# Optimization experiments

Measured on AMD Instinct MI355X. Metric: run time of the kernel, lower is better.

The kernel has to match this reference:

```python
import jax, jax.numpy as jnp
import numpy as np

SEQ_LEN = 2048; WIN = 32; NW = SEQ_LEN // WIN; FEAT = 16
H = 64; E = 128; NH = 4; OUT = 5; B = 256; MAXN = 2


def setup_inputs() -> dict:
    key = jax.random.key(0)
    ks = jax.random.split(key, 20)
    n = lambda k, shape, s=0.05: jax.random.normal(k, shape, dtype=jnp.float32) * s
    return {
        'x': n(ks[0], (B, SEQ_LEN, FEAT), 1.0),
        # bidirectional LSTM (torch gate order i,f,g,o)
        'w_ih_f': n(ks[1], (4 * H, FEAT)), 'w_hh_f': n(ks[2], (4 * H, H)),
        'b_ih_f': jnp.zeros((4 * H,)), 'b_hh_f': jnp.zeros((4 * H,)),
        'w_ih_b': n(ks[3], (4 * H, FEAT)), 'w_hh_b': n(ks[4], (4 * H, H)),
        'b_ih_b': jnp.zeros((4 * H,)), 'b_hh_b': jnp.zeros((4 * H,)),
        # self-attention on bi-LSTM output (embed_dim = 2H = E)
        'sa_in_w': n(ks[5], (3 * E, E)), 'sa_in_b': jnp.zeros((3 * E,)),
        'sa_out_w': n(ks[6], (E, E)), 'sa_out_b': jnp.zeros((E,)),
        # projection 2H -> embed_dim
        'proj_w': n(ks[7], (E, 2 * H)), 'proj_b': jnp.zeros((E,)),
        # per-window cross-attention blocks (stacked along NW)
        'ca_in_w': n(ks[8], (NW, 3 * E, E)), 'ca_in_b': jnp.zeros((NW, 3 * E)),
        'ca_out_w': n(ks[9], (NW, E, E)), 'ca_out_b': jnp.zeros((NW, E)),
        'ln_g': jnp.ones((NW, E)), 'ln_b': jnp.zeros((NW, E)),
        # final dense heads
        'fd1_w': n(ks[10], (64, E * NW)), 'fd1_b': jnp.zeros((64,)),
        'fd2_w': n(ks[11], (OUT, 64)), 'fd2_b': jnp.zeros((OUT,)),
    }


def _lstm_dir(x, w_ih, w_hh, b_ih, b_hh):
    # x: [N, T, F] -> hidden states [N, T, H]
    N = x.shape[0]
    Hh = w_hh.shape[1]
    xp = jnp.einsum('ntf,gf->ntg', x, w_ih) + b_ih + b_hh  # [N,T,4H]

    def step(carry, xt):
        h, c = carry
        g = xt + h @ w_hh.T
        i, f, gg, o = jnp.split(g, 4, axis=-1)
        i = jax.nn.sigmoid(i); f = jax.nn.sigmoid(f)
        gg = jnp.tanh(gg); o = jax.nn.sigmoid(o)
        c = f * c + i * gg
        h = o * jnp.tanh(c)
        return (h, c), h

    init = (jnp.zeros((N, Hh), x.dtype), jnp.zeros((N, Hh), x.dtype))
    _, hs = jax.lax.scan(step, init, jnp.swapaxes(xp, 0, 1))
    return jnp.swapaxes(hs, 0, 1)


def _bilstm(x, wif, whf, bif, bhf, wib, whb, bib, bhb):
    fwd = _lstm_dir(x, wif, whf, bif, bhf)
    bwd = _lstm_dir(x[:, ::-1], wib, whb, bib, bhb)[:, ::-1]
    return jnp.concatenate([fwd, bwd], axis=-1)  # [N, T, 2H]


def _mha(q_x, kv_x, in_w, in_b, out_w, out_b, nh):
    # torch nn.MultiheadAttention (batch_first, eval mode)
    Ed = q_x.shape[-1]; d = Ed // nh
    q = q_x @ in_w[:Ed].T + in_b[:Ed]
    k = kv_x @ in_w[Ed:2 * Ed].T + in_b[Ed:2 * Ed]
    v = kv_x @ in_w[2 * Ed:].T + in_b[2 * Ed:]
    sh = lambda t: t.reshape(t.shape[0], t.shape[1], nh, d)
    q, k, v = sh(q), sh(k), sh(v)
    s = jnp.einsum('nqhd,nkhd->nhqk', q, k) / jnp.asarray(np.sqrt(d), q.dtype)
    a = jax.nn.softmax(s, axis=-1)
    o = jnp.einsum('nhqk,nkhd->nqhd', a, v).reshape(q_x.shape[0], q_x.shape[1], Ed)
    return o @ out_w.T + out_b


def _layernorm(x, g, b, eps=1e-5):
    m = x.mean(-1, keepdims=True)
    v = ((x - m) ** 2).mean(-1, keepdims=True)
    return (x - m) / jnp.sqrt(v + eps) * g + b


def reference(x, w_ih_f, w_hh_f, b_ih_f, b_hh_f, w_ih_b, w_hh_b, b_ih_b, b_hh_b,
              sa_in_w, sa_in_b, sa_out_w, sa_out_b, proj_w, proj_b,
              ca_in_w, ca_in_b, ca_out_w, ca_out_b, ln_g, ln_b,
              fd1_w, fd1_b, fd2_w, fd2_b):
    Bsz = x.shape[0]
    xw = x[:, :NW * WIN].reshape(Bsz * NW, WIN, FEAT)
    # bi-LSTM + self-attention (dropout = identity in eval)
    lo = _bilstm(xw, w_ih_f, w_hh_f, b_ih_f, b_hh_f, w_ih_b, w_hh_b, b_ih_b, b_hh_b)
    sa = _mha(lo, lo, sa_in_w, sa_in_b, sa_out_w, sa_out_b, NH)
    p = sa @ proj_w.T + proj_b
    pooled = p.mean(axis=1).reshape(Bsz, NW, E)
    # per-window local cross-attention with distinct weights per window
    outs = []
    for ci in range(NW):
        left = max(0, ci - MAXN); right = min(NW, ci + MAXN + 1)
        idx = np.array([i for i in range(left, right) if i != ci])
        ctx = pooled[:, idx, :]           # [B, <=2*MAXN, E]
        cen = pooled[:, ci:ci + 1, :]     # [B, 1, E]
        a = _mha(cen, ctx, ca_in_w[ci], ca_in_b[ci], ca_out_w[ci], ca_out_b[ci], NH)
        outs.append(_layernorm(a + cen, ln_g[ci], ln_b[ci]))
    seq = jnp.concatenate(outs, axis=1).reshape(Bsz, NW * E)
    h1 = jax.nn.relu(seq @ fd1_w.T + fd1_b)
    out = h1 @ fd2_w.T + fd2_b            # [B, OUT]
    return out
```

## Files before the change

### kernel.cpp

```cpp
#include <hip/hip_runtime.h>


typedef __attribute__((ext_vector_type(8))) short bf16x8;
typedef __attribute__((ext_vector_type(4))) float f32x4;

__device__ __forceinline__ unsigned short f2bf(float f) {
    union { float f; unsigned int u; } v; v.f = f;
    unsigned int u = v.u;
    return (unsigned short)((u + 0x7FFFu + ((u >> 16) & 1u)) >> 16);
}
__device__ __forceinline__ float dot4_(float4 a, float4 b) {
    return a.x*b.x + a.y*b.y + a.z*b.z + a.w*b.w;
}
__device__ __forceinline__ bf16x8 f2bf8(float4 a, float4 b) {
    bf16x8 o;
    o[0] = (short)f2bf(a.x); o[1] = (short)f2bf(a.y);
    o[2] = (short)f2bf(a.z); o[3] = (short)f2bf(a.w);
    o[4] = (short)f2bf(b.x); o[5] = (short)f2bf(b.y);
    o[6] = (short)f2bf(b.z); o[7] = (short)f2bf(b.w);
    return o;
}
__device__ __forceinline__ float bflo(unsigned u){ union{unsigned u;float f;}v; v.u=u<<16; return v.f; }
__device__ __forceinline__ float bfhi(unsigned u){ union{unsigned u;float f;}v; v.u=u&0xffff0000u; return v.f; }
#define KEEP(f) { uint4* _p = (uint4*)&(f); \
    asm volatile("" : "+v"(_p->x), "+v"(_p->y), "+v"(_p->z), "+v"(_p->w)); }

#define W_SA_IN   0
#define W_SA_OUT  49152
#define W_PROJ    65536
#define W_IH_F    81920
#define W_IH_B    86016
#define W_HH_F    90112
#define W_HH_B    106496
#define W_CA_IN   122880
#define W_CA_OUT  3268608
#define NBF_SMALL 122880
#define NBF_FULL  4317184

__global__ __launch_bounds__(256)
void prep_weights(const float* __restrict__ sa_in_w, const float* __restrict__ sa_out_w,
                  const float* __restrict__ proj_w,
                  const float* __restrict__ w_ih_f, const float* __restrict__ w_ih_b,
                  const float* __restrict__ w_hh_f, const float* __restrict__ w_hh_b,
                  const float* __restrict__ ca_in_w, const float* __restrict__ ca_out_w,
                  unsigned short* __restrict__ wbf, int n)
{
    for (int i = blockIdx.x * 256 + threadIdx.x; i < n; i += gridDim.x * 256) {
        float v;
        if (i < W_SA_OUT)       v = sa_in_w[i];
        else if (i < W_PROJ)    v = sa_out_w[i - W_SA_OUT];
        else if (i < W_IH_F)    v = proj_w[i - W_PROJ];
        else if (i < W_IH_B)    v = w_ih_f[i - W_IH_F];
        else if (i < W_HH_F)    v = w_ih_b[i - W_IH_B];
        else if (i < W_HH_B)    v = w_hh_f[i - W_HH_F];
        else if (i < W_CA_IN)   v = w_hh_b[i - W_HH_B];
        else if (i < W_CA_OUT)  v = ca_in_w[i - W_CA_IN];
        else                    v = ca_out_w[i - W_CA_OUT];
        wbf[i] = f2bf(v);
    }
}

__global__ __launch_bounds__(128)
void prep_w2(const float* __restrict__ sa_out_w, const float* __restrict__ sa_out_b,
             const float* __restrict__ proj_w, const float* __restrict__ proj_b,
             unsigned short* __restrict__ w2bf, float* __restrict__ b2f)
{
    __shared__ float pw[128];
    const int e = blockIdx.x, j = threadIdx.x;
    pw[j] = proj_w[e * 128 + j];
    __syncthreads();
    float acc = 0.f;
    #pragma unroll 8
    for (int k = 0; k < 128; ++k) acc += pw[k] * sa_out_w[k * 128 + j];
    w2bf[e * 128 + j] = f2bf(acc);
    if (j == 0) {
        float b = proj_b[e];
        for (int k = 0; k < 128; ++k) b += pw[k] * sa_out_b[k];
        b2f[e] = b;
    }
}

#define HB 0
#define XS 9216
#define LSTM_SM 25856

__global__ __launch_bounds__(512)
void lstm_kernel(const float* __restrict__ x,
    const float* __restrict__ b_ih_f, const float* __restrict__ b_hh_f,
    const float* __restrict__ b_ih_b, const float* __restrict__ b_hh_b,
    const unsigned short* __restrict__ wbf,
    unsigned short* __restrict__ lo, int win0)
{
    __shared__ __align__(16) unsigned short sm[LSTM_SM];
    const int tid = threadIdx.x;
    const int gbase = win0 + blockIdx.x * 32;
    const int bb = gbase >> 6;
    const int wi0 = gbase & 63;

    for (int i = tid; i < 9216; i += 512) sm[HB + i] = 0;
    #pragma unroll
    for (int i = 0; i < 2; ++i) {
        const int p = tid + i * 512;
        const int win = p >> 5, t = p & 31;
        const float4* src = (const float4*)(x + ((size_t)bb * 2048 + (wi0 + win) * 32 + t) * 16);
        const float4 v0 = src[0], v1 = src[1], v2 = src[2], v3 = src[3];
        *(bf16x8*)&sm[XS + win * 520 + t * 16]     = f2bf8(v0, v1);
        *(bf16x8*)&sm[XS + win * 520 + t * 16 + 8] = f2bf8(v2, v3);
    }
    __syncthreads();

    const int w = tid >> 6, lane = tid & 63;
    const int dir = w >> 2, wd = w & 3;
    const int quad = lane >> 4, n16 = lane & 15;
    const bf16x8 zf = {};

    const unsigned short* whh = wbf + (dir ? W_HH_B : W_HH_F);
    const unsigned short* wih = wbf + (dir ? W_IH_B : W_IH_F);
    const float* bi = dir ? b_ih_b : b_ih_f;
    const float* bh = dir ? b_hh_b : b_hh_f;

    bf16x8 wf[4][2], xf[4];
    float bias[4];
    #pragma unroll
    for (int j = 0; j < 4; ++j) {
        const int g = 64 * j + wd * 16 + n16;
        wf[j][0] = *(const bf16x8*)(whh + g * 64 + quad * 8);
        wf[j][1] = *(const bf16x8*)(whh + g * 64 + 32 + quad * 8);
        KEEP(wf[j][0]); KEEP(wf[j][1]);
        xf[j] = (quad < 2) ? *(const bf16x8*)(wih + g * 16 + quad * 8) : zf;
        KEEP(xf[j]);
        bias[j] = bi[g] + bh[g];
    }
    float c[2][4] = {};
    const size_t loB = (size_t)blockIdx.x * 32;

    for (int s = 0; s < 32; ++s) {
        const int t = dir ? (31 - s) : s;
        const int cur = s & 1, nxt = cur ^ 1;
        #pragma unroll
        for (int mt = 0; mt < 2; ++mt) {
            const int hb = HB + ((cur * 2 + dir) * 32 + mt * 16 + n16) * 72;
            const bf16x8 ah0 = *(const bf16x8*)&sm[hb + quad * 8];
            const bf16x8 ah1 = *(const bf16x8*)&sm[hb + 32 + quad * 8];
            const bf16x8 ax = (quad < 2)
                ? *(const bf16x8*)&sm[XS + (mt * 16 + n16) * 520 + t * 16 + quad * 8] : zf;
            f32x4 ga[4];
            #pragma unroll
            for (int j = 0; j < 4; ++j) {
                f32x4 acc = {bias[j], bias[j], bias[j], bias[j]};
                acc = __builtin_amdgcn_mfma_f32_16x16x32_bf16(ah0, wf[j][0], acc, 0, 0, 0);
                acc = __builtin_amdgcn_mfma_f32_16x16x32_bf16(ah1, wf[j][1], acc, 0, 0, 0);
                acc = __builtin_amdgcn_mfma_f32_16x16x32_bf16(ax,  xf[j],   acc, 0, 0, 0);
                ga[j] = acc;
            }
            #pragma unroll
            for (int r = 0; r < 4; ++r) {
                const float iv = 1.f / (1.f + __expf(-ga[0][r]));
                const float fv = 1.f / (1.f + __expf(-ga[1][r]));
                const float gv = 2.f / (1.f + __expf(-2.f * ga[2][r])) - 1.f;
                const float ov = 1.f / (1.f + __expf(-ga[3][r]));
                c[mt][r] = fv * c[mt][r] + iv * gv;
                const float hv = ov * (2.f / (1.f + __expf(-2.f * c[mt][r])) - 1.f);
                sm[HB + ((nxt * 2 + dir) * 32 + mt * 16 + quad * 4 + r) * 72 + wd * 16 + n16]
                    = f2bf(hv);
            }
        }
        __syncthreads();
        {
            const int win = tid >> 4, part = tid & 15;
            const int d2 = part >> 3, u0 = (part & 7) * 8;
            const int t2 = d2 ? (31 - s) : s;
            const uint4 hv = *(const uint4*)&sm[HB + ((nxt * 2 + d2) * 32 + win) * 72 + u0];
            *(uint4*)(lo + ((loB + win) * 32 + t2) * 128 + d2 * 64 + u0) = hv;
        }
    }
}

#define LO16 0
#define Q16  4352
#define K16  8704
#define VT16 13056
#define SM16_TOTAL 18176

__global__ __launch_bounds__(512)
void attn_kernel(const unsigned short* __restrict__ wbf,
    const float* __restrict__ sa_in_b,
    const unsigned short* __restrict__ w2bf, const float* __restrict__ b2f,
    const unsigned short* __restrict__ lo,
    float* __restrict__ pooled, int win0)
{
    __shared__ __align__(16) unsigned short sm16[SM16_TOTAL];
    const int tid = threadIdx.x;

    {
        const uint4 v = *(const uint4*)(lo + (size_t)blockIdx.x * 4096 + tid * 8);
        const int t = tid >> 4, e0 = (tid & 15) * 8;
        *(uint4*)&sm16[LO16 + t * 136 + e0] = v;
    }
    __syncthreads();

    const int w    = tid >> 6;
    const int lane = tid & 63;
    const int quad = lane >> 4;
    const int m16  = lane & 15;
    const unsigned short* wqkv = wbf + W_SA_IN;
    const f32x4 z = {0.f, 0.f, 0.f, 0.f};

    {
        bf16x8 afr[2][4];
        #pragma unroll
        for (int mt = 0; mt < 2; ++mt)
            #pragma unroll
            for (int kk = 0; kk < 4; ++kk)
                afr[mt][kk] = *(const bf16x8*)&sm16[LO16 + (mt*16 + m16)*136 + kk*32 + quad*8];
        #pragma unroll
        for (int i = 0; i < 3; ++i) {
            const int nt = w * 3 + i;
            const int e = nt * 16 + m16;
            bf16x8 bfr[4];
            #pragma unroll
            for (int kk = 0; kk < 4; ++kk)
                bfr[kk] = *(const bf16x8*)(wqkv + (size_t)e*128 + kk*32 + quad*8);
            f32x4 acc0 = z, acc1 = z;
            #pragma unroll
            for (int kk = 0; kk < 4; ++kk) {
                acc0 = __builtin_amdgcn_mfma_f32_16x16x32_bf16(afr[0][kk], bfr[kk], acc0, 0, 0, 0);
                acc1 = __builtin_amdgcn_mfma_f32_16x16x32_bf16(afr[1][kk], bfr[kk], acc1, 0, 0, 0);
            }
            const float bias = sa_in_b[e];
            #pragma unroll
            for (int r = 0; r < 4; ++r) {
                const int r0 = quad*4 + r, r1 = 16 + r0;
                const unsigned short h0 = f2bf(acc0[r] + bias);
                const unsigned short h1 = f2bf(acc1[r] + bias);
                if (e < 128) {
                    sm16[Q16 + r0*136 + e] = h0;
                    sm16[Q16 + r1*136 + e] = h1;
                } else if (e < 256) {
                    sm16[K16 + r0*136 + (e-128)] = h0;
                    sm16[K16 + r1*136 + (e-128)] = h1;
                } else {
                    sm16[VT16 + (e-256)*40 + r0] = h0;
                    sm16[VT16 + (e-256)*40 + r1] = h1;
                }
            }
        }
    }
    __syncthreads();

    {
        const int h  = w >> 1;
        const int mt = w & 1;
        const bf16x8 aq  = *(const bf16x8*)&sm16[Q16 + (mt*16 + m16)*136 + h*32 + quad*8];
        const bf16x8 bk0 = *(const bf16x8*)&sm16[K16 + (m16)*136      + h*32 + quad*8];
        const bf16x8 bk1 = *(const bf16x8*)&sm16[K16 + (16 + m16)*136 + h*32 + quad*8];
        f32x4 s0 = __builtin_amdgcn_mfma_f32_16x16x32_bf16(aq, bk0, z, 0, 0, 0);
        f32x4 s1 = __builtin_amdgcn_mfma_f32_16x16x32_bf16(aq, bk1, z, 0, 0, 0);
        const float scale = 0.17677669529663687f;
        #pragma unroll
        for (int r = 0; r < 4; ++r) {
            const int rowt = mt*16 + quad*4 + r;
            sm16[Q16 + rowt*136 + h*32 + m16]      = f2bf(__expf(s0[r] * scale));
            sm16[Q16 + rowt*136 + h*32 + 16 + m16] = f2bf(__expf(s1[r] * scale));
        }
        const bf16x8 ap  = *(const bf16x8*)&sm16[Q16 + (mt*16 + m16)*136 + h*32 + quad*8];
        bf16x8 ones;
        #pragma unroll
        for (int j = 0; j < 8; ++j) ones[j] = (short)0x3F80;
        const f32x4 sums = __builtin_amdgcn_mfma_f32_16x16x32_bf16(ap, ones, z, 0, 0, 0);
        const bf16x8 bv0 = *(const bf16x8*)&sm16[VT16 + (h*32 + m16)*40      + quad*8];
        const bf16x8 bv1 = *(const bf16x8*)&sm16[VT16 + (h*32 + 16 + m16)*40 + quad*8];
        f32x4 o0 = __builtin_amdgcn_mfma_f32_16x16x32_bf16(ap, bv0, z, 0, 0, 0);
        f32x4 o1 = __builtin_amdgcn_mfma_f32_16x16x32_bf16(ap, bv1, z, 0, 0, 0);
        float cs0 = 0.f, cs1 = 0.f;
        #pragma unroll
        for (int r = 0; r < 4; ++r) {
            const float inv = 1.f / sums[r];
            cs0 += o0[r] * inv;
            cs1 += o1[r] * inv;
        }
        cs0 += __shfl_xor(cs0, 16, 64); cs0 += __shfl_xor(cs0, 32, 64);
        cs1 += __shfl_xor(cs1, 16, 64); cs1 += __shfl_xor(cs1, 32, 64);
        float* osum = (float*)&sm16[LO16];
        if (quad == 0) {
            osum[mt*128 + h*32 + m16]      = cs0;
            osum[mt*128 + h*32 + 16 + m16] = cs1;
        }
    }
    __syncthreads();

    if (tid < 128) {
        const float* osum = (const float*)&sm16[LO16];
        float acc = b2f[tid];
        const unsigned short* wrow = w2bf + tid * 128;
        #pragma unroll
        for (int j0 = 0; j0 < 128; j0 += 8) {
            const uint4 u = *(const uint4*)(wrow + j0);
            acc += (osum[j0+0] + osum[128+j0+0]) * 0.03125f * bflo(u.x);
            acc += (osum[j0+1] + osum[128+j0+1]) * 0.03125f * bfhi(u.x);
            acc += (osum[j0+2] + osum[128+j0+2]) * 0.03125f * bflo(u.y);
            acc += (osum[j0+3] + osum[128+j0+3]) * 0.03125f * bfhi(u.y);
            acc += (osum[j0+4] + osum[128+j0+4]) * 0.03125f * bflo(u.z);
            acc += (osum[j0+5] + osum[128+j0+5]) * 0.03125f * bfhi(u.z);
            acc += (osum[j0+6] + osum[128+j0+6]) * 0.03125f * bflo(u.w);
            acc += (osum[j0+7] + osum[128+j0+7]) * 0.03125f * bfhi(u.w);
        }
        pooled[((size_t)(win0 + blockIdx.x)) * 128 + tid] = acc;
    }
}

__global__ __launch_bounds__(256)
void cross_mfma_kernel(const float* __restrict__ pooled,
    const unsigned short* __restrict__ wbf,
    const float* __restrict__ ca_in_b, const float* __restrict__ ca_out_b,
    const float* __restrict__ ln_g, const float* __restrict__ ln_b,
    float* __restrict__ seq)
{
    __shared__ __align__(16) float cenf[16 * 128];
    __shared__ __align__(16) unsigned short cenb[16 * 136];
    __shared__ __align__(16) unsigned short ctxb[64 * 136];
    __shared__ __align__(16) unsigned short qb[16 * 136];
    __shared__ __align__(16) unsigned short kb[64 * 136];
    __shared__ __align__(16) unsigned short ob[16 * 136];
    __shared__ float attr[256];
    __shared__ float att[256];

    const int blk = blockIdx.x;
    const int ci = blk >> 4;
    const int ch = blk & 15;
    const int tid = threadIdx.x;
    const int w = tid >> 6, lane = tid & 63, quad = lane >> 4, n16 = lane & 15;

    const int left  = (ci - 2 > 0) ? ci - 2 : 0;
    const int right = (ci + 3 < 64) ? ci + 3 : 64;
    const int nc = right - left - 1;

    {
        const int b = tid >> 4, e0 = (tid & 15) * 8;
        const float4* src = (const float4*)(pooled + ((size_t)(ch*16 + b)*64 + ci)*128 + e0);
        const float4 v0 = src[0], v1 = src[1];
        *(float4*)&cenf[b*128 + e0]     = v0;
        *(float4*)&cenf[b*128 + e0 + 4] = v1;
        *(bf16x8*)&cenb[b*136 + e0] = f2bf8(v0, v1);
        for (int n2 = 0; n2 < nc; ++n2) {
            int idx = left + n2; if (idx >= ci) idx++;
            const float4* s2 = (const float4*)(pooled + ((size_t)(ch*16 + b)*64 + idx)*128 + e0);
            *(bf16x8*)&ctxb[(n2*16 + b)*136 + e0] = f2bf8(s2[0], s2[1]);
        }
    }
    __syncthreads();

    const unsigned short* wi = wbf + W_CA_IN + (size_t)ci * 49152;

    #pragma unroll
    for (int i = 0; i < 2; ++i) {
        const int nt = w + i * 4;
        const int e = nt * 16 + n16;
        {
            const float bq = ca_in_b[ci*384 + e];
            f32x4 acc = {bq, bq, bq, bq};
            #pragma unroll
            for (int kk = 0; kk < 4; ++kk) {
                const bf16x8 a = *(const bf16x8*)&cenb[n16*136 + kk*32 + quad*8];
                const bf16x8 bfr = *(const bf16x8*)(wi + (size_t)e*128 + kk*32 + quad*8);
                acc = __builtin_amdgcn_mfma_f32_16x16x32_bf16(a, bfr, acc, 0, 0, 0);
            }
            #pragma unroll
            for (int r = 0; r < 4; ++r) qb[(quad*4 + r)*136 + e] = f2bf(acc[r]);
        }
        {
            bf16x8 bk[4];
            #pragma unroll
            for (int kk = 0; kk < 4; ++kk)
                bk[kk] = *(const bf16x8*)(wi + (size_t)(128 + e)*128 + kk*32 + quad*8);
            const float bkb = ca_in_b[ci*384 + 128 + e];
            for (int mt = 0; mt < nc; ++mt) {
                f32x4 acc = {bkb, bkb, bkb, bkb};
                #pragma unroll
                for (int kk = 0; kk < 4; ++kk) {
                    const bf16x8 a = *(const bf16x8*)&ctxb[(mt*16 + n16)*136 + kk*32 + quad*8];
                    acc = __builtin_amdgcn_mfma_f32_16x16x32_bf16(a, bk[kk], acc, 0, 0, 0);
                }
                #pragma unroll
                for (int r = 0; r < 4; ++r) kb[(mt*16 + quad*4 + r)*136 + e] = f2bf(acc[r]);
            }
        }
    }
    __syncthreads();

    {
        const int h = w;
        const bf16x8 aq = *(const bf16x8*)&qb[n16*136 + h*32 + quad*8];
        for (int n2 = 0; n2 < nc; ++n2) {
            const bf16x8 bk = *(const bf16x8*)&kb[(n2*16 + n16)*136 + h*32 + quad*8];
            const f32x4 z = {0.f, 0.f, 0.f, 0.f};
            const f32x4 s = __builtin_amdgcn_mfma_f32_16x16x32_bf16(aq, bk, z, 0, 0, 0);
            if ((n16 >> 2) == quad)
                attr[(h*4 + n2)*16 + n16] = s[n16 & 3] * 0.17677669529663687f;
        }
    }
    __syncthreads();

    if (tid < 64) {
        const int b = tid & 15, h = tid >> 4;
        float m = -1e30f;
        for (int n2 = 0; n2 < nc; ++n2) m = fmaxf(m, attr[(h*4 + n2)*16 + b]);
        float e2[4]; float sum = 0.f;
        for (int n2 = 0; n2 < nc; ++n2) { e2[n2] = __expf(attr[(h*4 + n2)*16 + b] - m); sum += e2[n2]; }
        const float inv = 1.f / sum;
        for (int n2 = 0; n2 < nc; ++n2) att[b*16 + h*4 + n2] = e2[n2] * inv;
    }
    __syncthreads();

    #pragma unroll
    for (int i = 0; i < 2; ++i) {
        const int nt = w + i * 4;
        const int e = nt * 16 + n16;
        const int he = nt >> 1;
        bf16x8 bv[4];
        #pragma unroll
        for (int kk = 0; kk < 4; ++kk)
            bv[kk] = *(const bf16x8*)(wi + (size_t)(256 + e)*128 + kk*32 + quad*8);
        const float bvb = ca_in_b[ci*384 + 256 + e];
        float accO[4] = {bvb, bvb, bvb, bvb};
        for (int mt = 0; mt < nc; ++mt) {
            f32x4 vv = {0.f, 0.f, 0.f, 0.f};
            #pragma unroll
            for (int kk = 0; kk < 4; ++kk) {
                const bf16x8 a = *(const bf16x8*)&ctxb[(mt*16 + n16)*136 + kk*32 + quad*8];
                vv = __builtin_amdgcn_mfma_f32_16x16x32_bf16(a, bv[kk], vv, 0, 0, 0);
            }
            #pragma unroll
            for (int r = 0; r < 4; ++r)
                accO[r] += att[(quad*4 + r)*16 + he*4 + mt] * vv[r];
        }
        #pragma unroll
        for (int r = 0; r < 4; ++r) ob[(quad*4 + r)*136 + e] = f2bf(accO[r]);
    }
    __syncthreads();

    const unsigned short* wo = wbf + W_CA_OUT + (size_t)ci * 16384;
    float* resf = (float*)ctxb;
    #pragma unroll
    for (int i = 0; i < 2; ++i) {
        const int nt = w + i * 4;
        const int e = nt * 16 + n16;
        const float bo = ca_out_b[ci*128 + e];
        f32x4 acc = {bo, bo, bo, bo};
        #pragma unroll
        for (int kk = 0; kk < 4; ++kk) {
            const bf16x8 a = *(const bf16x8*)&ob[n16*136 + kk*32 + quad*8];
            const bf16x8 bfr = *(const bf16x8*)(wo + (size_t)e*128 + kk*32 + quad*8);
            acc = __builtin_amdgcn_mfma_f32_16x16x32_bf16(a, bfr, acc, 0, 0, 0);
        }
        #pragma unroll
        for (int r = 0; r < 4; ++r) {
            const int b2 = quad*4 + r;
            resf[b2*128 + e] = acc[r] + cenf[b2*128 + e];
        }
    }
    __syncthreads();

    {
        const int b = tid >> 4, i16 = tid & 15;
        const float4 v0 = *(float4*)&resf[b*128 + i16*8];
        const float4 v1 = *(float4*)&resf[b*128 + i16*8 + 4];
        float sum = v0.x+v0.y+v0.z+v0.w + v1.x+v1.y+v1.z+v1.w;
        float sq = v0.x*v0.x+v0.y*v0.y+v0.z*v0.z+v0.w*v0.w
                 + v1.x*v1.x+v1.y*v1.y+v1.z*v1.z+v1.w*v1.w;
        #pragma unroll
        for (int msk = 1; msk < 16; msk <<= 1) {
            sum += __shfl_xor(sum, msk, 64);
            sq  += __shfl_xor(sq, msk, 64);
        }
        const float mean = sum * (1.f / 128.f);
        const float var = sq * (1.f / 128.f) - mean * mean;
        const float rstd = rsqrtf(var + 1e-5f);
        float* dst = seq + ((size_t)(ch*16 + b)*64 + ci)*128 + i16*8;
        const float* gp = ln_g + ci*128 + i16*8;
        const float* bp = ln_b + ci*128 + i16*8;
        float4 o0, o1;
        o0.x = (v0.x-mean)*rstd*gp[0]+bp[0]; o0.y = (v0.y-mean)*rstd*gp[1]+bp[1];
        o0.z = (v0.z-mean)*rstd*gp[2]+bp[2]; o0.w = (v0.w-mean)*rstd*gp[3]+bp[3];
        o1.x = (v1.x-mean)*rstd*gp[4]+bp[4]; o1.y = (v1.y-mean)*rstd*gp[5]+bp[5];
        o1.z = (v1.z-mean)*rstd*gp[6]+bp[6]; o1.w = (v1.w-mean)*rstd*gp[7]+bp[7];
        *(float4*)dst = o0;
        *(float4*)(dst + 4) = o1;
    }
}

__global__ __launch_bounds__(512)
void fused_window_kernel(const float* __restrict__ x,
    const float* __restrict__ w_ih_f, const float* __restrict__ w_hh_f,
    const float* __restrict__ b_ih_f, const float* __restrict__ b_hh_f,
    const float* __restrict__ w_ih_b, const float* __restrict__ w_hh_b,
    const float* __restrict__ b_ih_b, const float* __restrict__ b_hh_b,
    const float* __restrict__ sa_in_b, const float* __restrict__ sa_out_b,
    const float* __restrict__ proj_b,
    const unsigned short* __restrict__ wbf,
    float* __restrict__ pooled)
{
    __shared__ __align__(16) unsigned short sm16[SM16_TOTAL];
    float* xs   = (float*)&sm16[VT16];
    float* hbuf = xs + 512;
    const int tid = threadIdx.x;
    const int blk = blockIdx.x;
    const int bb = blk >> 6, wi2 = blk & 63;
    {
        const float* xsrc = x + ((size_t)bb * 2048 + wi2 * 32) * 16;
        xs[tid & 511] = xsrc[tid];
        if (tid < 256) hbuf[tid] = 0.f;
    }
    __syncthreads();
    {
        const int dir  = tid >> 8;
        const int gg   = tid & 255;
        const int u    = gg >> 2;
        const int gate = gg & 3;
        const int row  = gate * 64 + u;
        const float4* wih_p = (const float4*)((dir ? w_ih_b : w_ih_f) + row * 16);
        const float4* whh_p = (const float4*)((dir ? w_hh_b : w_hh_f) + row * 64);
        float4 wih[4];
        #pragma unroll
        for (int i = 0; i < 4; ++i) wih[i] = wih_p[i];
        float4 whh[16];
        #pragma unroll
        for (int i = 0; i < 16; ++i) whh[i] = whh_p[i];
        const float bias = dir ? (b_ih_b[row] + b_hh_b[row]) : (b_ih_f[row] + b_hh_f[row]);
        const float km  = (gate == 2) ? 2.f : 1.f;
        const float ofs = (gate == 2) ? -1.f : 0.f;
        const int qb2 = (tid & 63) & ~3;
        float c = 0.f;
        for (int step = 0; step < 32; ++step) {
            const int t = dir ? (31 - step) : step;
            const float4* h4 = (const float4*)&hbuf[(step & 1) * 128 + dir * 64];
            const float4* x4 = (const float4*)&xs[t * 16];
            float a0 = bias, a1 = 0.f, a2 = 0.f, a3 = 0.f;
            #pragma unroll
            for (int j = 0; j < 16; j += 4) {
                a0 += dot4_(h4[j], whh[j]);     a1 += dot4_(h4[j+1], whh[j+1]);
                a2 += dot4_(h4[j+2], whh[j+2]); a3 += dot4_(h4[j+3], whh[j+3]);
            }
            a0 += dot4_(x4[0], wih[0]); a1 += dot4_(x4[1], wih[1]);
            a2 += dot4_(x4[2], wih[2]); a3 += dot4_(x4[3], wih[3]);
            const float acc = (a0 + a1) + (a2 + a3);
            const float act = km / (1.f + __expf(-km * acc)) + ofs;
            const float iv = __shfl(act, qb2 + 0, 64);
            const float fv = __shfl(act, qb2 + 1, 64);
            const float gv = __shfl(act, qb2 + 2, 64);
            const float ov = __shfl(act, qb2 + 3, 64);
            c = fv * c + iv * gv;
            const float h = ov * (2.f / (1.f + __expf(-2.f * c)) - 1.f);
            if (gate == 0) {
                hbuf[((step + 1) & 1) * 128 + dir * 64 + u] = h;
                sm16[LO16 + t * 136 + dir * 64 + u] = f2bf(h);
            }
            __syncthreads();
        }
    }
    const int w = tid >> 6, lane = tid & 63, quad = lane >> 4, m16 = lane & 15;
    const unsigned short* wqkv = wbf + W_SA_IN;
    const unsigned short* wout = wbf + W_SA_OUT;
    const unsigned short* wprj = wbf + W_PROJ;
    {
        const int mt = w & 1, ng = w >> 1;
        bf16x8 afr[4];
        #pragma unroll
        for (int kk = 0; kk < 4; ++kk)
            afr[kk] = *(const bf16x8*)&sm16[LO16 + (mt*16 + m16)*136 + kk*32 + quad*8];
        #pragma unroll
        for (int i = 0; i < 6; ++i) {
            const int nt = ng * 6 + i;
            f32x4 acc = {0.f, 0.f, 0.f, 0.f};
            #pragma unroll
            for (int kk = 0; kk < 4; ++kk) {
                const bf16x8 bfr = *(const bf16x8*)(wqkv + (nt*16 + m16)*128 + kk*32 + quad*8);
                acc = __builtin_amdgcn_mfma_f32_16x16x32_bf16(afr[kk], bfr, acc, 0, 0, 0);
            }
            const int e = nt * 16 + m16;
            const float bias = sa_in_b[e];
            #pragma unroll
            for (int r = 0; r < 4; ++r) {
                const int rowt = mt*16 + quad*4 + r;
                const unsigned short hv = f2bf(acc[r] + bias);
                if (e < 128)       sm16[Q16 + rowt*136 + e] = hv;
                else if (e < 256)  sm16[K16 + rowt*136 + (e - 128)] = hv;
                else               sm16[VT16 + (e - 256)*40 + rowt] = hv;
            }
        }
    }
    __syncthreads();
    {
        const int h = w >> 1, mt = w & 1;
        const bf16x8 aq  = *(const bf16x8*)&sm16[Q16 + (mt*16 + m16)*136 + h*32 + quad*8];
        const bf16x8 bk0 = *(const bf16x8*)&sm16[K16 + (m16)*136      + h*32 + quad*8];
        const bf16x8 bk1 = *(const bf16x8*)&sm16[K16 + (16 + m16)*136 + h*32 + quad*8];
        __syncthreads();
        const f32x4 z = {0.f, 0.f, 0.f, 0.f};
        f32x4 s0 = __builtin_amdgcn_mfma_f32_16x16x32_bf16(aq, bk0, z, 0, 0, 0);
        f32x4 s1 = __builtin_amdgcn_mfma_f32_16x16x32_bf16(aq, bk1, z, 0, 0, 0);
        const float scale = 0.17677669529663687f;
        #pragma unroll
        for (int r = 0; r < 4; ++r) {
            float v0 = s0[r] * scale, v1 = s1[r] * scale;
            float mx = fmaxf(v0, v1);
            #pragma unroll
            for (int msk = 1; msk < 16; msk <<= 1) mx = fmaxf(mx, __shfl_xor(mx, msk, 64));
            const float e0 = __expf(v0 - mx), e1 = __expf(v1 - mx);
            float sum = e0 + e1;
            #pragma unroll
            for (int msk = 1; msk < 16; msk <<= 1) sum += __shfl_xor(sum, msk, 64);
            const float inv = 1.f / sum;
            const int rowt = mt*16 + quad*4 + r;
            sm16[Q16 + rowt*136 + h*32 + m16]      = f2bf(e0 * inv);
            sm16[Q16 + rowt*136 + h*32 + 16 + m16] = f2bf(e1 * inv);
        }
        const bf16x8 ap  = *(const bf16x8*)&sm16[Q16 + (mt*16 + m16)*136 + h*32 + quad*8];
        const bf16x8 bv0 = *(const bf16x8*)&sm16[VT16 + (h*32 + m16)*40      + quad*8];
        const bf16x8 bv1 = *(const bf16x8*)&sm16[VT16 + (h*32 + 16 + m16)*40 + quad*8];
        f32x4 o0 = __builtin_amdgcn_mfma_f32_16x16x32_bf16(ap, bv0, z, 0, 0, 0);
        f32x4 o1 = __builtin_amdgcn_mfma_f32_16x16x32_bf16(ap, bv1, z, 0, 0, 0);
        #pragma unroll
        for (int r = 0; r < 4; ++r) {
            const int rowt = mt*16 + quad*4 + r;
            sm16[K16 + rowt*136 + h*32 + m16]      = f2bf(o0[r]);
            sm16[K16 + rowt*136 + h*32 + 16 + m16] = f2bf(o1[r]);
        }
    }
    __syncthreads();
    {
        const int mt = w & 1;
        bf16x8 ao[4];
        #pragma unroll
        for (int kk = 0; kk < 4; ++kk)
            ao[kk] = *(const bf16x8*)&sm16[K16 + (mt*16 + m16)*136 + kk*32 + quad*8];
        #pragma unroll
        for (int i = 0; i < 2; ++i) {
            const int nt = (w >> 1) * 2 + i;
            f32x4 acc = {0.f, 0.f, 0.f, 0.f};
            #pragma unroll
            for (int kk = 0; kk < 4; ++kk) {
                const bf16x8 bfr = *(const bf16x8*)(wout + (nt*16 + m16)*128 + kk*32 + quad*8);
                acc = __builtin_amdgcn_mfma_f32_16x16x32_bf16(ao[kk], bfr, acc, 0, 0, 0);
            }
            const int e = nt * 16 + m16;
            const float bias = sa_out_b[e];
            #pragma unroll
            for (int r = 0; r < 4; ++r)
                sm16[LO16 + (mt*16 + quad*4 + r)*136 + e] = f2bf(acc[r] + bias);
        }
    }
    __syncthreads();
    {
        f32x4 acc0 = {0.f, 0.f, 0.f, 0.f};
        f32x4 acc1 = {0.f, 0.f, 0.f, 0.f};
        #pragma unroll
        for (int kk = 0; kk < 4; ++kk) {
            const bf16x8 a0 = *(const bf16x8*)&sm16[LO16 + (m16)*136      + kk*32 + quad*8];
            const bf16x8 a1 = *(const bf16x8*)&sm16[LO16 + (16 + m16)*136 + kk*32 + quad*8];
            const bf16x8 bfr = *(const bf16x8*)(wprj + (w*16 + m16)*128 + kk*32 + quad*8);
            acc0 = __builtin_amdgcn_mfma_f32_16x16x32_bf16(a0, bfr, acc0, 0, 0, 0);
            acc1 = __builtin_amdgcn_mfma_f32_16x16x32_bf16(a1, bfr, acc1, 0, 0, 0);
        }
        float s = (acc0[0] + acc0[1]) + (acc0[2] + acc0[3])
                + (acc1[0] + acc1[1]) + (acc1[2] + acc1[3]);
        s += __shfl_down(s, 32, 64);
        s += __shfl_down(s, 16, 64);
        if (lane < 16) {
            const int e = w * 16 + lane;
            pooled[(size_t)blk * 128 + e] = s * 0.03125f + proj_b[e];
        }
    }
}

__global__ __launch_bounds__(128)
void cross_attn_kernel(const float* __restrict__ pooled,
    const float* __restrict__ ca_in_w, const float* __restrict__ ca_in_b,
    const float* __restrict__ ca_out_w, const float* __restrict__ ca_out_b,
    const float* __restrict__ ln_g, const float* __restrict__ ln_b,
    float* __restrict__ seq)
{
    const int blk = blockIdx.x;
    const int ci = blk >> 8, bb = blk & 255;
    const int tid = threadIdx.x;
    __shared__ float cen[128], ctx[512], qsh[128], ksh[512], vsh[512], osh[128];
    __shared__ float att2[16], red[2];
    const int left  = (ci - 2 > 0) ? ci - 2 : 0;
    const int right = (ci + 3 < 64) ? ci + 3 : 64;
    const int nc = right - left - 1;
    cen[tid] = pooled[((size_t)bb * 64 + ci) * 128 + tid];
    for (int n2 = 0; n2 < nc; ++n2) {
        int idx = left + n2; if (idx >= ci) idx++;
        ctx[n2 * 128 + tid] = pooled[((size_t)bb * 64 + idx) * 128 + tid];
    }
    __syncthreads();
    const float* Wi = ca_in_w + (size_t)ci * 384 * 128;
    const float* bi = ca_in_b + ci * 384;
    const int e = tid;
    {
        const float4* wr = (const float4*)(Wi + (size_t)e * 128);
        const float4* cr = (const float4*)cen;
        float acc = bi[e];
        #pragma unroll 8
        for (int j = 0; j < 32; ++j) acc += dot4_(cr[j], wr[j]);
        qsh[e] = acc;
    }
    for (int n2 = 0; n2 < nc; ++n2) {
        const float4* xr = (const float4*)&ctx[n2 * 128];
        const float4* wk = (const float4*)(Wi + (size_t)(128 + e) * 128);
        const float4* wv = (const float4*)(Wi + (size_t)(256 + e) * 128);
        float acck = bi[128 + e], accv = bi[256 + e];
        #pragma unroll 8
        for (int j = 0; j < 32; ++j) {
            const float4 a = xr[j];
            acck += dot4_(a, wk[j]); accv += dot4_(a, wv[j]);
        }
        ksh[n2 * 128 + e] = acck; vsh[n2 * 128 + e] = accv;
    }
    __syncthreads();
    if (tid < 4) {
        const int h = tid;
        float s[4]; float m = -1e30f;
        for (int n2 = 0; n2 < nc; ++n2) {
            float acc = 0.f;
            #pragma unroll
            for (int d = 0; d < 32; ++d) acc += qsh[h*32 + d] * ksh[n2*128 + h*32 + d];
            s[n2] = acc * 0.17677669529663687f;
            m = fmaxf(m, s[n2]);
        }
        float ssum = 0.f;
        for (int n2 = 0; n2 < nc; ++n2) { s[n2] = __expf(s[n2] - m); ssum += s[n2]; }
        const float inv = 1.f / ssum;
        for (int n2 = 0; n2 < nc; ++n2) att2[h*4 + n2] = s[n2] * inv;
    }
    __syncthreads();
    {
        const int h = e >> 5;
        float oacc = 0.f;
        for (int n2 = 0; n2 < nc; ++n2) oacc += att2[h*4 + n2] * vsh[n2*128 + e];
        osh[e] = oacc;
    }
    __syncthreads();
    float res;
    {
        const float4* wr = (const float4*)(ca_out_w + (size_t)ci*128*128 + (size_t)e*128);
        const float4* orow = (const float4*)osh;
        float acc = ca_out_b[ci*128 + e];
        #pragma unroll 8
        for (int j = 0; j < 32; ++j) acc += dot4_(orow[j], wr[j]);
        res = acc + cen[e];
    }
    const int lane = tid & 63, wid = tid >> 6;
    float sum = res;
    #pragma unroll
    for (int off = 32; off > 0; off >>= 1) sum += __shfl_down(sum, off, 64);
    if (lane == 0) red[wid] = sum;
    __syncthreads();
    const float mean = (red[0] + red[1]) * (1.f / 128.f);
    const float dv = res - mean;
    __syncthreads();
    float s2 = dv * dv;
    #pragma unroll
    for (int off = 32; off > 0; off >>= 1) s2 += __shfl_down(s2, off, 64);
    if (lane == 0) red[wid] = s2;
    __syncthreads();
    const float var = (red[0] + red[1]) * (1.f / 128.f);
    const float y = dv * rsqrtf(var + 1e-5f) * ln_g[ci*128 + e] + ln_b[ci*128 + e];
    seq[((size_t)bb * 64 + ci) * 128 + e] = y;
}

__global__ __launch_bounds__(1024)
void head_kernel(const float* __restrict__ seq,
    const float* __restrict__ fd1_w, const float* __restrict__ fd1_b,
    const float* __restrict__ fd2_w, const float* __restrict__ fd2_b,
    float* __restrict__ out)
{
    const int bb = blockIdx.x;
    const int tid = threadIdx.x;
    const int j = tid >> 4, part = tid & 15;
    __shared__ float red[1024];
    __shared__ float h1[64];
    float acc = 0.f;
    const float4* wr = (const float4*)(fd1_w + (size_t)j * 8192 + part * 512);
    const float4* sr = (const float4*)(seq + (size_t)bb * 8192 + part * 512);
    #pragma unroll 4
    for (int i = 0; i < 128; ++i) acc += dot4_(sr[i], wr[i]);
    red[tid] = acc;
    __syncthreads();
    if (tid < 64) {
        float s = fd1_b[tid];
        #pragma unroll
        for (int p = 0; p < 16; ++p) s += red[tid * 16 + p];
        h1[tid] = fmaxf(s, 0.f);
    }
    __syncthreads();
    if (tid < 5) {
        float acc2 = fd2_b[tid];
        const float* w2 = fd2_w + tid * 64;
        #pragma unroll
        for (int k = 0; k < 64; ++k) acc2 += h1[k] * w2[k];
        out[bb * 5 + tid] = acc2;
    }
}

extern "C" void kernel_launch(void* const* d_in, const int* in_sizes, int n_in,
                              void* d_out, int out_size, void* d_ws, size_t ws_size,
                              hipStream_t stream) {
    const float* x        = (const float*)d_in[0];
    const float* w_ih_f   = (const float*)d_in[1];
    const float* w_hh_f   = (const float*)d_in[2];
    const float* b_ih_f   = (const float*)d_in[3];
    const float* b_hh_f   = (const float*)d_in[4];
    const float* w_ih_b   = (const float*)d_in[5];
    const float* w_hh_b   = (const float*)d_in[6];
    const float* b_ih_b   = (const float*)d_in[7];
    const float* b_hh_b   = (const float*)d_in[8];
    const float* sa_in_w  = (const float*)d_in[9];
    const float* sa_in_b  = (const float*)d_in[10];
    const float* sa_out_w = (const float*)d_in[11];
    const float* sa_out_b = (const float*)d_in[12];
    const float* proj_w   = (const float*)d_in[13];
    const float* proj_b   = (const float*)d_in[14];
    const float* ca_in_w  = (const float*)d_in[15];
    const float* ca_in_b  = (const float*)d_in[16];
    const float* ca_out_w = (const float*)d_in[17];
    const float* ca_out_b = (const float*)d_in[18];
    const float* ln_g     = (const float*)d_in[19];
    const float* ln_b     = (const float*)d_in[20];
    const float* fd1_w    = (const float*)d_in[21];
    const float* fd1_b    = (const float*)d_in[22];
    const float* fd2_w    = (const float*)d_in[23];
    const float* fd2_b    = (const float*)d_in[24];

    float* pooled = (float*)d_ws;
    float* seq    = pooled + 2097152;
    float* outp   = (float*)d_out;

    const size_t base = 2ull * 8388608 + 8634368;
    const size_t loFull = 134217728ull;

    if (ws_size >= base + loFull / 4) {
        unsigned short* wbf = (unsigned short*)((char*)d_ws + 16777216);
        unsigned short* lo  = (unsigned short*)((char*)d_ws + base);
        unsigned short* w2bf = (unsigned short*)seq;
        float* b2f = (float*)(w2bf + 16384);
        const int npass = (ws_size >= base + loFull) ? 1
                        : (ws_size >= base + loFull / 2) ? 2 : 4;
        prep_weights<<<dim3(2048), dim3(256), 0, stream>>>(
            sa_in_w, sa_out_w, proj_w, w_ih_f, w_ih_b, w_hh_f, w_hh_b,
            ca_in_w, ca_out_w, wbf, NBF_FULL);
        prep_w2<<<dim3(128), dim3(128), 0, stream>>>(
            sa_out_w, sa_out_b, proj_w, proj_b, w2bf, b2f);
        const int chunk = 16384 / npass;
        for (int p = 0; p < npass; ++p) {
            const int win0 = p * chunk;
            lstm_kernel<<<dim3(chunk / 32), dim3(512), 0, stream>>>(
                x, b_ih_f, b_hh_f, b_ih_b, b_hh_b, wbf, lo, win0);
            attn_kernel<<<dim3(chunk), dim3(512), 0, stream>>>(
                wbf, sa_in_b, w2bf, b2f, lo, pooled, win0);
        }
        cross_mfma_kernel<<<dim3(1024), dim3(256), 0, stream>>>(
            pooled, wbf, ca_in_b, ca_out_b, ln_g, ln_b, seq);
    } else {
        unsigned short* wbf = (unsigned short*)seq;
        prep_weights<<<dim3(2048), dim3(256), 0, stream>>>(
            sa_in_w, sa_out_w, proj_w, w_ih_f, w_ih_b, w_hh_f, w_hh_b,
            ca_in_w, ca_out_w, wbf, NBF_SMALL);
        fused_window_kernel<<<dim3(16384), dim3(512), 0, stream>>>(
            x, w_ih_f, w_hh_f, b_ih_f, b_hh_f, w_ih_b, w_hh_b, b_ih_b, b_hh_b,
            sa_in_b, sa_out_b, proj_b, wbf, pooled);
        cross_attn_kernel<<<dim3(16384), dim3(128), 0, stream>>>(
            pooled, ca_in_w, ca_in_b, ca_out_w, ca_out_b, ln_g, ln_b, seq);
    }

    head_kernel<<<dim3(256), dim3(1024), 0, stream>>>(
        seq, fd1_w, fd1_b, fd2_w, fd2_b, outp);
}
```

Baseline: 700.4 us.

## Reuse fd1 weights across four samples in head; spread attn tail over all threads

```diff
diff --git a/kernel.cpp b/kernel.cpp
--- a/kernel.cpp
+++ b/kernel.cpp
@@ -215,7 +215,7 @@
                 afr[mt][kk] = *(const bf16x8*)&sm16[LO16 + (mt*16 + m16)*136 + kk*32 + quad*8];
         #pragma unroll
         for (int i = 0; i < 3; ++i) {
-            const int nt = w * 3 + i;
+            const int nt = w + i * 8;
             const int e = nt * 16 + m16;
             bf16x8 bfr[4];
             #pragma unroll
@@ -228,20 +228,28 @@
                 acc1 = __builtin_amdgcn_mfma_f32_16x16x32_bf16(afr[1][kk], bfr[kk], acc1, 0, 0, 0);
             }
             const float bias = sa_in_b[e];
-            #pragma unroll
-            for (int r = 0; r < 4; ++r) {
-                const int r0 = quad*4 + r, r1 = 16 + r0;
-                const unsigned short h0 = f2bf(acc0[r] + bias);
-                const unsigned short h1 = f2bf(acc1[r] + bias);
-                if (e < 128) {
-                    sm16[Q16 + r0*136 + e] = h0;
-                    sm16[Q16 + r1*136 + e] = h1;
-                } else if (e < 256) {
-                    sm16[K16 + r0*136 + (e-128)] = h0;
-                    sm16[K16 + r1*136 + (e-128)] = h1;
-                } else {
-                    sm16[VT16 + (e-256)*40 + r0] = h0;
-                    sm16[VT16 + (e-256)*40 + r1] = h1;
+            if (i == 0) {
+                #pragma unroll
+                for (int r = 0; r < 4; ++r) {
+                    const int r0 = quad*4 + r;
+                    sm16[Q16 + r0*136 + e]        = f2bf(acc0[r] + bias);
+                    sm16[Q16 + (16 + r0)*136 + e] = f2bf(acc1[r] + bias);
+                }
+            } else if (i == 1) {
+                const int ek = e - 128;
+                #pragma unroll
+                for (int r = 0; r < 4; ++r) {
+                    const int r0 = quad*4 + r;
+                    sm16[K16 + r0*136 + ek]        = f2bf(acc0[r] + bias);
+                    sm16[K16 + (16 + r0)*136 + ek] = f2bf(acc1[r] + bias);
+                }
+            } else {
+                const int ev = e - 256;
+                #pragma unroll
+                for (int r = 0; r < 4; ++r) {
+                    const int r0 = quad*4 + r;
+                    sm16[VT16 + ev*40 + r0]      = f2bf(acc0[r] + bias);
+                    sm16[VT16 + ev*40 + 16 + r0] = f2bf(acc1[r] + bias);
                 }
             }
         }
@@ -289,23 +297,32 @@
     }
     __syncthreads();
 
-    if (tid < 128) {
+    {
         const float* osum = (const float*)&sm16[LO16];
-        float acc = b2f[tid];
-        const unsigned short* wrow = w2bf + tid * 128;
-        #pragma unroll
-        for (int j0 = 0; j0 < 128; j0 += 8) {
-            const uint4 u = *(const uint4*)(wrow + j0);
-            acc += (osum[j0+0] + osum[128+j0+0]) * 0.03125f * bflo(u.x);
-            acc += (osum[j0+1] + osum[128+j0+1]) * 0.03125f * bfhi(u.x);
-            acc += (osum[j0+2] + osum[128+j0+2]) * 0.03125f * bflo(u.y);
-            acc += (osum[j0+3] + osum[128+j0+3]) * 0.03125f * bfhi(u.y);
-            acc += (osum[j0+4] + osum[128+j0+4]) * 0.03125f * bflo(u.z);
-            acc += (osum[j0+5] + osum[128+j0+5]) * 0.03125f * bfhi(u.z);
-            acc += (osum[j0+6] + osum[128+j0+6]) * 0.03125f * bflo(u.w);
-            acc += (osum[j0+7] + osum[128+j0+7]) * 0.03125f * bfhi(u.w);
-        }
-        pooled[((size_t)(win0 + blockIdx.x)) * 128 + tid] = acc;
+        const int e = tid >> 2, part = tid & 3;
+        const int k0 = part * 32;
+        float acc = 0.f;
+        const unsigned short* wrow = w2bf + e * 128 + k0;
+        #pragma unroll
+        for (int j = 0; j < 32; j += 8) {
+            const float4 a0 = *(const float4*)&osum[k0 + j];
+            const float4 a1 = *(const float4*)&osum[k0 + j + 4];
+            const float4 b0 = *(const float4*)&osum[128 + k0 + j];
+            const float4 b1 = *(const float4*)&osum[128 + k0 + j + 4];
+            const uint4 u = *(const uint4*)(wrow + j);
+            acc += (a0.x + b0.x) * bflo(u.x);
+            acc += (a0.y + b0.y) * bfhi(u.x);
+            acc += (a0.z + b0.z) * bflo(u.y);
+            acc += (a0.w + b0.w) * bfhi(u.y);
+            acc += (a1.x + b1.x) * bflo(u.z);
+            acc += (a1.y + b1.y) * bfhi(u.z);
+            acc += (a1.z + b1.z) * bflo(u.w);
+            acc += (a1.w + b1.w) * bfhi(u.w);
+        }
+        acc += __shfl_xor(acc, 1, 64);
+        acc += __shfl_xor(acc, 2, 64);
+        if (part == 0)
+            pooled[((size_t)(win0 + blockIdx.x)) * 128 + e] = acc * 0.03125f + b2f[e];
     }
 }
 
@@ -486,6 +503,56 @@
         o1.z = (v1.z-mean)*rstd*gp[6]+bp[6]; o1.w = (v1.w-mean)*rstd*gp[7]+bp[7];
         *(float4*)dst = o0;
         *(float4*)(dst + 4) = o1;
+    }
+}
+
+__global__ __launch_bounds__(1024)
+void head_kernel(const float* __restrict__ seq,
+    const float* __restrict__ fd1_w, const float* __restrict__ fd1_b,
+    const float* __restrict__ fd2_w, const float* __restrict__ fd2_b,
+    float* __restrict__ out)
+{
+    const int bb4 = blockIdx.x;
+    const int tid = threadIdx.x;
+    const int j = tid >> 4, part = tid & 15;
+    __shared__ float4 red[1024];
+    __shared__ float h1[4][64];
+    float a0 = 0.f, a1 = 0.f, a2 = 0.f, a3 = 0.f;
+    const float4* wr = (const float4*)(fd1_w + (size_t)j * 8192 + part * 512);
+    const float4* s0 = (const float4*)(seq + ((size_t)bb4*4 + 0) * 8192 + part * 512);
+    const float4* s1 = (const float4*)(seq + ((size_t)bb4*4 + 1) * 8192 + part * 512);
+    const float4* s2 = (const float4*)(seq + ((size_t)bb4*4 + 2) * 8192 + part * 512);
+    const float4* s3 = (const float4*)(seq + ((size_t)bb4*4 + 3) * 8192 + part * 512);
+    #pragma unroll 4
+    for (int i = 0; i < 128; ++i) {
+        const float4 w4 = wr[i];
+        a0 += dot4_(s0[i], w4);
+        a1 += dot4_(s1[i], w4);
+        a2 += dot4_(s2[i], w4);
+        a3 += dot4_(s3[i], w4);
+    }
+    red[tid] = make_float4(a0, a1, a2, a3);
+    __syncthreads();
+    if (tid < 64) {
+        float t0 = fd1_b[tid], t1 = t0, t2 = t0, t3 = t0;
+        #pragma unroll
+        for (int p = 0; p < 16; ++p) {
+            const float4 v = red[tid * 16 + p];
+            t0 += v.x; t1 += v.y; t2 += v.z; t3 += v.w;
+        }
+        h1[0][tid] = fmaxf(t0, 0.f);
+        h1[1][tid] = fmaxf(t1, 0.f);
+        h1[2][tid] = fmaxf(t2, 0.f);
+        h1[3][tid] = fmaxf(t3, 0.f);
+    }
+    __syncthreads();
+    if (tid < 20) {
+        const int r = tid / 5, o = tid % 5;
+        float acc2 = fd2_b[o];
+        const float* w2 = fd2_w + o * 64;
+        #pragma unroll
+        for (int k = 0; k < 64; ++k) acc2 += h1[r][k] * w2[k];
+        out[(bb4 * 4 + r) * 5 + o] = acc2;
     }
 }
 
@@ -767,40 +834,6 @@
     const float var = (red[0] + red[1]) * (1.f / 128.f);
     const float y = dv * rsqrtf(var + 1e-5f) * ln_g[ci*128 + e] + ln_b[ci*128 + e];
     seq[((size_t)bb * 64 + ci) * 128 + e] = y;
-}
-
-__global__ __launch_bounds__(1024)
-void head_kernel(const float* __restrict__ seq,
-    const float* __restrict__ fd1_w, const float* __restrict__ fd1_b,
-    const float* __restrict__ fd2_w, const float* __restrict__ fd2_b,
-    float* __restrict__ out)
-{
-    const int bb = blockIdx.x;
-    const int tid = threadIdx.x;
-    const int j = tid >> 4, part = tid & 15;
-    __shared__ float red[1024];
-    __shared__ float h1[64];
-    float acc = 0.f;
-    const float4* wr = (const float4*)(fd1_w + (size_t)j * 8192 + part * 512);
-    const float4* sr = (const float4*)(seq + (size_t)bb * 8192 + part * 512);
-    #pragma unroll 4
-    for (int i = 0; i < 128; ++i) acc += dot4_(sr[i], wr[i]);
-    red[tid] = acc;
-    __syncthreads();
-    if (tid < 64) {
-        float s = fd1_b[tid];
-        #pragma unroll
-        for (int p = 0; p < 16; ++p) s += red[tid * 16 + p];
-        h1[tid] = fmaxf(s, 0.f);
-    }
-    __syncthreads();
-    if (tid < 5) {
-        float acc2 = fd2_b[tid];
-        const float* w2 = fd2_w + tid * 64;
-        #pragma unroll
-        for (int k = 0; k < 64; ++k) acc2 += h1[k] * w2[k];
-        out[bb * 5 + tid] = acc2;
-    }
 }
 
 extern "C" void kernel_launch(void* const* d_in, const int* in_sizes, int n_in,
@@ -873,6 +906,6 @@
             pooled, ca_in_w, ca_in_b, ca_out_w, ca_out_b, ln_g, ln_b, seq);
     }
 
-    head_kernel<<<dim3(256), dim3(1024), 0, stream>>>(
+    head_kernel<<<dim3(64), dim3(1024), 0, stream>>>(
         seq, fd1_w, fd1_b, fd2_w, fd2_b, outp);
 }
```

New measurement: 836.9 us. 1.2x slower.
